# Kernel optimization log

Measured on AMD Instinct MI355X. Metric: run time of the kernel, lower is better.

The kernel has to match this reference:

```python
import jax, jax.numpy as jnp
import numpy as np

K_DIM = 1024
HEADS = 16


def setup_inputs() -> dict:
    key = jax.random.key(0)
    ks = jax.random.split(key, 6)
    b, t, k = 2, 2048, K_DIM
    scale = 1.0 / np.sqrt(k)
    x = jax.random.normal(ks[0], (b, t, k), dtype=jnp.float32)
    # nn.Linear stores weight as [out, in]; y = x @ W.T
    Wq = jax.random.normal(ks[1], (k, k), dtype=jnp.float32) * scale
    Wk = jax.random.normal(ks[2], (k, k), dtype=jnp.float32) * scale
    Wv = jax.random.normal(ks[3], (k, k), dtype=jnp.float32) * scale
    Wo = jax.random.normal(ks[4], (k, k), dtype=jnp.float32) * scale
    bo = jax.random.normal(ks[5], (k,), dtype=jnp.float32) * scale
    return {"x": x, "Wq": Wq, "Wk": Wk, "Wv": Wv, "Wo": Wo, "bo": bo}


def reference(x, Wq, Wk, Wv, Wo, bo):
    b, t, k = x.shape
    h = HEADS
    hd = k // h
    q = (x @ Wq.T).reshape(b, t, h, hd)
    kk = (x @ Wk.T).reshape(b, t, h, hd)
    v = (x @ Wv.T).reshape(b, t, h, hd)
    # scores: [b, h, t, t]
    scores = jnp.einsum('bqhd,bkhd->bhqk', q, kk) / jnp.sqrt(jnp.float32(hd))
    w = jax.nn.softmax(scores, axis=-1)
    out = jnp.einsum('bhqk,bkhd->bqhd', w, v).reshape(b, t, k)
    return out @ Wo.T + bo
```

## Files before the change

kernel.cpp:

```cpp
#include <hip/hip_runtime.h>
#include <stdint.h>
#include <stddef.h>

#define TB 2048
#define KDIM 1024
#define NH 16
#define HD 64

typedef __attribute__((ext_vector_type(8))) __bf16 bf16x8;
typedef __attribute__((ext_vector_type(2))) float f32x2;
typedef __attribute__((ext_vector_type(4))) float f32x4;
typedef __attribute__((ext_vector_type(16))) float f32x16;
typedef __attribute__((ext_vector_type(4))) unsigned short u16x4;
typedef __attribute__((ext_vector_type(8))) unsigned short u16x8;
typedef __attribute__((ext_vector_type(4))) unsigned u32x4;
typedef __attribute__((ext_vector_type(2))) unsigned u32x2;

static __device__ __forceinline__ unsigned short f2bf(float f) {
  unsigned u = __builtin_bit_cast(unsigned, f);
  return (unsigned short)((u + 0x7FFFu + ((u >> 16) & 1u)) >> 16);
}

static __device__ __forceinline__ bf16x8 ld_frag(const unsigned short* p) {
  u16x8 v = *(const u16x8*)p;
  return __builtin_bit_cast(bf16x8, v);
}

static __device__ __forceinline__ void gload_lds16(const void* g, void* l) {
  auto gp = (const __attribute__((address_space(1))) unsigned int*)(uintptr_t)g;
  auto lp = (__attribute__((address_space(3))) unsigned int*)(unsigned int)(uintptr_t)l;
  __builtin_amdgcn_global_load_lds(gp, lp, 16, 0, 0);
}

static __device__ __forceinline__ float fast_exp2(float x) {
  float r;
  asm("v_exp_f32 %0, %1" : "=v"(r) : "v"(x));
  return r;
}

static __device__ __forceinline__ unsigned cvt_pk(float a, float b) {
  unsigned r;
  asm("v_cvt_pk_bf16_f32 %0, %1, %2" : "=v"(r) : "v"(a), "v"(b));
  return r;
}

static __device__ __forceinline__ u32x2 permswap(unsigned a, unsigned b) {
  return __builtin_amdgcn_permlane32_swap(a, b, false, false);
}

static __device__ __forceinline__ f32x2 pk_fma(f32x2 a, f32x2 b, f32x2 c) {
  f32x2 d;
  asm("v_pk_fma_f32 %0, %1, %2, %3" : "=v"(d) : "v"(a), "v"(b), "v"(c));
  return d;
}
static __device__ __forceinline__ f32x2 pk_add(f32x2 a, f32x2 b) {
  f32x2 d;
  asm("v_pk_add_f32 %0, %1, %2" : "=v"(d) : "v"(a), "v"(b));
  return d;
}

__global__ __launch_bounds__(256) void k_cvt_all(
    const float* __restrict__ x, const float* __restrict__ Wq,
    const float* __restrict__ Wk, const float* __restrict__ Wv,
    const float* __restrict__ Wo, unsigned short* __restrict__ xb,
    unsigned short* __restrict__ wb) {
  int bb = blockIdx.x;
  const float* src;
  unsigned short* dst;
  int i;
  if (bb < 2048) {
    src = x; dst = xb; i = bb * 256 + threadIdx.x;
  } else {
    int wsel = (bb - 2048) >> 9;
    src = (wsel == 0) ? Wq : (wsel == 1) ? Wk : (wsel == 2) ? Wv : Wo;
    dst = wb + (size_t)wsel * (KDIM * KDIM);
    i = ((bb - 2048) & 511) * 256 + threadIdx.x;
  }
  const float4* p = (const float4*)src + (size_t)i * 2;
  float4 a = p[0], b = p[1];
  u16x8 o;
  o[0] = f2bf(a.x); o[1] = f2bf(a.y); o[2] = f2bf(a.z); o[3] = f2bf(a.w);
  o[4] = f2bf(b.x); o[5] = f2bf(b.y); o[6] = f2bf(b.z); o[7] = f2bf(b.w);
  *((u16x8*)dst + i) = o;
}

template <int MODE>
static __device__ __forceinline__ void gemm_body(
    const unsigned short* __restrict__ A, const unsigned short* __restrict__ W,
    unsigned short* __restrict__ Cb, float* __restrict__ Cf,
    const float* __restrict__ bias, int by, int bx,
    unsigned short* As, unsigned short* Bs) {
  const int K = KDIM, N = KDIM;
  int tid = threadIdx.x, lane = tid & 63, wid = tid >> 6;
  int r = lane & 15, g = lane >> 4;
  int wm = wid >> 1, wn = wid & 1;

  f32x4 acc[4][4];
#pragma unroll
  for (int m = 0; m < 4; ++m)
#pragma unroll
    for (int n = 0; n < 4; ++n) acc[m][n] = (f32x4){0.f, 0.f, 0.f, 0.f};

  const unsigned short* Ag = A + (size_t)(by * 128) * K;
  const unsigned short* Wg = W + (size_t)(bx * 128) * K;

  for (int k0 = 0; k0 < K; k0 += 64) {
#pragma unroll
    for (int it = 0; it < 4; ++it) {
      int base = it * 256 + wid * 64;
      int c = base + lane;
      int rr = c >> 3;
      int blk = (c & 7) ^ (rr & 7);
      gload_lds16(Ag + (size_t)rr * K + k0 + blk * 8, &As[base * 8]);
      gload_lds16(Wg + (size_t)rr * K + k0 + blk * 8, &Bs[base * 8]);
    }
    __syncthreads();
#pragma unroll
    for (int ks = 0; ks < 2; ++ks) {
      bf16x8 af[4], bf[4];
#pragma unroll
      for (int m = 0; m < 4; ++m) {
        int row = wm * 64 + m * 16 + r;
        af[m] = ld_frag(&As[row * 64 + ((ks * 4 + g) ^ (r & 7)) * 8]);
      }
#pragma unroll
      for (int n = 0; n < 4; ++n) {
        int row = wn * 64 + n * 16 + r;
        bf[n] = ld_frag(&Bs[row * 64 + ((ks * 4 + g) ^ (r & 7)) * 8]);
      }
      __builtin_amdgcn_s_setprio(1);
#pragma unroll
      for (int m = 0; m < 4; ++m)
#pragma unroll
        for (int n = 0; n < 4; ++n)
          acc[m][n] = __builtin_amdgcn_mfma_f32_16x16x32_bf16(af[m], bf[n], acc[m][n], 0, 0, 0);
      __builtin_amdgcn_s_setprio(0);
    }
    __syncthreads();
  }

#pragma unroll
  for (int m = 0; m < 4; ++m)
#pragma unroll
    for (int n = 0; n < 4; ++n) {
      int col = bx * 128 + wn * 64 + n * 16 + r;
      if (MODE == 2) {
        int hq = col >> 6, dq = col & 63;
        int row0 = by * 128 + wm * 64 + m * 16 + g * 4;
        int bq = row0 >> 11, tq = row0 & 2047;
        u16x4 pv;
#pragma unroll
        for (int j = 0; j < 4; ++j) pv[j] = f2bf(acc[m][n][j]);
        *(u16x4*)&Cb[(((size_t)(bq * NH + hq)) * HD + dq) * TB + tq] = pv;
      } else {
#pragma unroll
        for (int j = 0; j < 4; ++j) {
          int row = by * 128 + wm * 64 + m * 16 + g * 4 + j;
          if (MODE == 0)
            Cb[(size_t)row * N + col] = f2bf(acc[m][n][j]);
          else
            Cf[(size_t)row * N + col] = acc[m][n][j] + bias[col];
        }
      }
    }
}

__global__ __launch_bounds__(256) void k_gemm_qkv(
    const unsigned short* __restrict__ X,
    const unsigned short* __restrict__ Wq, const unsigned short* __restrict__ Wk,
    const unsigned short* __restrict__ Wv,
    unsigned short* __restrict__ Q, unsigned short* __restrict__ Kp,
    unsigned short* __restrict__ Vt) {
  __shared__ __align__(16) unsigned short As[8192];
  __shared__ __align__(16) unsigned short Bs[8192];
  int bidx = blockIdx.x;
  int xcd = bidx & 7, slot = bidx >> 3;
  int by = xcd * 4 + slot / 24;
  int bxx = slot % 24;
  int which = bxx >> 3, bx = bxx & 7;
  if (which == 2) {
    gemm_body<2>(X, Wv, Vt, nullptr, nullptr, by, bx, As, Bs);
  } else {
    const unsigned short* W = which ? Wk : Wq;
    unsigned short* C = which ? Kp : Q;
    gemm_body<0>(X, W, C, nullptr, nullptr, by, bx, As, Bs);
  }
}

__global__ __launch_bounds__(256) void k_gemm_out(
    const unsigned short* __restrict__ AO, const unsigned short* __restrict__ Wo,
    float* __restrict__ out, const float* __restrict__ bias) {
  __shared__ __align__(16) unsigned short As[8192];
  __shared__ __align__(16) unsigned short Bs[8192];
  int bidx = blockIdx.x;
  int xcd = bidx & 7, slot = bidx >> 3;
  int by = xcd * 4 + slot / 8;
  int bx = slot & 7;
  gemm_body<1>(AO, Wo, nullptr, out, bias, by, bx, As, Bs);
}

__global__ __launch_bounds__(512, 4) void k_attn(
    const unsigned short* __restrict__ Q, const unsigned short* __restrict__ Kp,
    const unsigned short* __restrict__ Vt, unsigned short* __restrict__ AO) {
  __shared__ __align__(16) unsigned short LDSb[6 * 4096];
  unsigned short* KsB = LDSb;
  unsigned short* VsB = LDSb + 3 * 4096;

  int qt = blockIdx.x >> 5, bh = blockIdx.x & 31;
  int b = bh >> 4, h = bh & 15;
  int tid = threadIdx.x, lane = tid & 63, w = tid >> 6;
  int wl = w & 3, kh = w >> 2;
  int q = lane & 31, hh = lane >> 5;
  const float LOG2E = 1.44269504f;
  const int NT = TB / 64;

  const unsigned short* Qp =
      Q + ((size_t)(b * TB + qt * 128 + wl * 32 + q)) * KDIM + h * HD;
  bf16x8 qf[4];
#pragma unroll
  for (int f = 0; f < 4; ++f) qf[f] = ld_frag(&Qp[16 * f + 8 * hh]);

  f32x16 o0, o1;
#pragma unroll
  for (int i = 0; i < 16; ++i) { o0[i] = 0.f; o1[i] = 0.f; }
  float l_run = 0.f;

  int c = w * 64 + lane;
  int rr = c >> 3;
  int blk = (c & 7) ^ (rr & 7);
  const unsigned short* Kg =
      Kp + (size_t)(b * TB) * KDIM + h * HD + (size_t)rr * KDIM + blk * 8;
  const unsigned short* Vg =
      Vt + (size_t)bh * HD * TB + (size_t)rr * TB + blk * 8;
  int ldst = w * 512;

  auto stage = [&](int kt, int buf) {
    gload_lds16(Kg + (size_t)kt * 64 * KDIM, &KsB[buf * 4096 + ldst]);
    gload_lds16(Vg + kt * 64, &VsB[buf * 4096 + ldst]);
  };

  stage(0, 0);
  stage(1, 1);
  asm volatile("s_waitcnt vmcnt(2)" ::: "memory");
  __builtin_amdgcn_s_barrier();
  __builtin_amdgcn_sched_barrier(0);

  const float c1 = 0.125f * LOG2E;
  const float c2 = 10.0f * LOG2E;
  f32x2 c1v; c1v[0] = c1; c1v[1] = c1;
  f32x2 c2v; c2v[0] = -c2; c2v[1] = -c2;

  for (int t = 0; t < NT; ++t) {
    int cur = t % 3;
    bool pf = (t + 2 < NT);
    if (pf) stage(t + 2, (t + 2) % 3);

    const unsigned short* Kc = &KsB[cur * 4096];
    f32x16 st;
#pragma unroll
    for (int i = 0; i < 16; ++i) st[i] = 0.f;
    __builtin_amdgcn_s_setprio(1);
#pragma unroll
    for (int f = 0; f < 4; ++f) {
      int row = kh * 32 + q;
      int bl = (2 * f + hh) ^ (q & 7);
      bf16x8 kf = ld_frag(&Kc[row * 64 + bl * 8]);
      st = __builtin_amdgcn_mfma_f32_32x32x16_bf16(kf, qf[f], st, 0, 0, 0);
    }
    __builtin_amdgcn_s_setprio(0);

    f32x2 rsv; rsv[0] = 0.f; rsv[1] = 0.f;
    unsigned d[8];
#pragma unroll
    for (int i = 0; i < 8; ++i) {
      f32x2 p; p[0] = st[2 * i]; p[1] = st[2 * i + 1];
      p = pk_fma(p, c1v, c2v);
      f32x2 e; e[0] = fast_exp2(p[0]); e[1] = fast_exp2(p[1]);
      rsv = pk_add(rsv, e);
      d[i] = cvt_pk(e[0], e[1]);
    }
    u32x2 r1 = permswap(d[0], d[2]);
    u32x2 r2 = permswap(d[1], d[3]);
    u32x2 r3 = permswap(d[4], d[6]);
    u32x2 r4 = permswap(d[5], d[7]);
    u32x4 t0; t0[0] = r1.x; t0[1] = r2.x; t0[2] = r1.y; t0[3] = r2.y;
    u32x4 t1; t1[0] = r3.x; t1[1] = r4.x; t1[2] = r3.y; t1[3] = r4.y;
    bf16x8 pa0 = __builtin_bit_cast(bf16x8, t0);
    bf16x8 pa1 = __builtin_bit_cast(bf16x8, t1);
    float rs = rsv[0] + rsv[1];
    rs += __shfl_xor(rs, 32);
    l_run += rs;

    const unsigned short* Vc = &VsB[cur * 4096];
    __builtin_amdgcn_s_setprio(1);
    {
      int bl0 = (kh * 4 + hh) ^ (q & 7);
      int bl1 = (kh * 4 + 2 + hh) ^ (q & 7);
      bf16x8 v00 = ld_frag(&Vc[q * 64 + bl0 * 8]);
      bf16x8 v01 = ld_frag(&Vc[(32 + q) * 64 + bl0 * 8]);
      bf16x8 v10 = ld_frag(&Vc[q * 64 + bl1 * 8]);
      bf16x8 v11 = ld_frag(&Vc[(32 + q) * 64 + bl1 * 8]);
      o0 = __builtin_amdgcn_mfma_f32_32x32x16_bf16(pa0, v00, o0, 0, 0, 0);
      o1 = __builtin_amdgcn_mfma_f32_32x32x16_bf16(pa0, v01, o1, 0, 0, 0);
      o0 = __builtin_amdgcn_mfma_f32_32x32x16_bf16(pa1, v10, o0, 0, 0, 0);
      o1 = __builtin_amdgcn_mfma_f32_32x32x16_bf16(pa1, v11, o1, 0, 0, 0);
    }
    __builtin_amdgcn_s_setprio(0);

    if (pf) asm volatile("s_waitcnt vmcnt(2)" ::: "memory");
    else    asm volatile("s_waitcnt vmcnt(0)" ::: "memory");
    __builtin_amdgcn_s_barrier();
    __builtin_amdgcn_sched_barrier(0);
  }

  float* Osw = (float*)LDSb;
  float* MLb = ((float*)LDSb) + 8192;
  if (kh) {
#pragma unroll
    for (int p = 0; p < 16; ++p) {
      Osw[p * 256 + wl * 64 + lane]        = o0[p];
      Osw[(16 + p) * 256 + wl * 64 + lane] = o1[p];
    }
    if (!hh) MLb[wl * 32 + q] = l_run;
  }
  __syncthreads();
  if (!kh) {
    float il = 1.f / (l_run + MLb[wl * 32 + q]);
#pragma unroll
    for (int p = 0; p < 16; ++p) {
      int qr = (p & 3) + 8 * (p >> 2) + 4 * hh;
      float ip = __shfl(il, qr);
      float v0 = (o0[p] + Osw[p * 256 + wl * 64 + lane]) * ip;
      float v1 = (o1[p] + Osw[(16 + p) * 256 + wl * 64 + lane]) * ip;
      int row = qt * 128 + wl * 32 + qr;
      size_t base = ((size_t)(b * TB + row)) * KDIM + h * HD;
      AO[base + q]      = f2bf(v0);
      AO[base + 32 + q] = f2bf(v1);
    }
  }
}

extern "C" void kernel_launch(void* const* d_in, const int* in_sizes, int n_in,
                              void* d_out, int out_size, void* d_ws, size_t ws_size,
                              hipStream_t stream) {
  const float* x  = (const float*)d_in[0];
  const float* Wq = (const float*)d_in[1];
  const float* Wk = (const float*)d_in[2];
  const float* Wv = (const float*)d_in[3];
  const float* Wo = (const float*)d_in[4];
  const float* bo = (const float*)d_in[5];

  char* ws = (char*)d_ws;
  const size_t MB = 1 << 20;
  unsigned short* xb  = (unsigned short*)(ws + 0 * MB);
  unsigned short* wqb = (unsigned short*)(ws + 8 * MB);
  unsigned short* wkb = (unsigned short*)(ws + 10 * MB);
  unsigned short* wvb = (unsigned short*)(ws + 12 * MB);
  unsigned short* wob = (unsigned short*)(ws + 14 * MB);
  unsigned short* Qb  = (unsigned short*)(ws + 16 * MB);
  unsigned short* Kb  = (unsigned short*)(ws + 24 * MB);
  unsigned short* Vtb = (unsigned short*)(ws + 32 * MB);
  unsigned short* AOb = (unsigned short*)(ws + 40 * MB);

  k_cvt_all<<<4096, 256, 0, stream>>>(x, Wq, Wk, Wv, Wo, xb, wqb);
  k_gemm_qkv<<<32 * 24, 256, 0, stream>>>(xb, wqb, wkb, wvb, Qb, Kb, Vtb);
  k_attn<<<512, 512, 0, stream>>>(Qb, Kb, Vtb, AOb);
  k_gemm_out<<<256, 256, 0, stream>>>(AOb, wob, (float*)d_out, bo);
}
```

Before: 114.0 us.

## Split attention KV range across two blocks and merge partials in a new kernel

The attention kernel now splits each (batch, head, query-tile) over two halves of the key sequence, launching 1024 blocks instead of 512. Each block writes unnormalised fp32 partial outputs and row sums to workspace, and a new merge kernel sums them, normalises and converts to bf16. This raises parallelism to fill more CUs and waves per CU, at the cost of extra global traffic for the partials and an additional launch. It relies on the softmax using a fixed max offset rather than a running max, so the partials can simply be added.

```diff
diff --git a/kernel.cpp b/kernel.cpp
--- a/kernel.cpp
+++ b/kernel.cpp
@@ -201,18 +201,21 @@
 
 __global__ __launch_bounds__(512, 4) void k_attn(
     const unsigned short* __restrict__ Q, const unsigned short* __restrict__ Kp,
-    const unsigned short* __restrict__ Vt, unsigned short* __restrict__ AO) {
+    const unsigned short* __restrict__ Vt,
+    float* __restrict__ Opart, float* __restrict__ lpart) {
   __shared__ __align__(16) unsigned short LDSb[6 * 4096];
   unsigned short* KsB = LDSb;
   unsigned short* VsB = LDSb + 3 * 4096;
 
-  int qt = blockIdx.x >> 5, bh = blockIdx.x & 31;
+  int bidx = blockIdx.x;
+  int bh = bidx & 31, qt = (bidx >> 5) & 15, half = bidx >> 9;
   int b = bh >> 4, h = bh & 15;
   int tid = threadIdx.x, lane = tid & 63, w = tid >> 6;
   int wl = w & 3, kh = w >> 2;
   int q = lane & 31, hh = lane >> 5;
   const float LOG2E = 1.44269504f;
-  const int NT = TB / 64;
+  const int NTH = 16;
+  int kt0 = half * NTH;
 
   const unsigned short* Qp =
       Q + ((size_t)(b * TB + qt * 128 + wl * 32 + q)) * KDIM + h * HD;
@@ -234,7 +237,8 @@
       Vt + (size_t)bh * HD * TB + (size_t)rr * TB + blk * 8;
   int ldst = w * 512;
 
-  auto stage = [&](int kt, int buf) {
+  auto stage = [&](int t, int buf) {
+    int kt = kt0 + t;
     gload_lds16(Kg + (size_t)kt * 64 * KDIM, &KsB[buf * 4096 + ldst]);
     gload_lds16(Vg + kt * 64, &VsB[buf * 4096 + ldst]);
   };
@@ -250,9 +254,9 @@
   f32x2 c1v; c1v[0] = c1; c1v[1] = c1;
   f32x2 c2v; c2v[0] = -c2; c2v[1] = -c2;
 
-  for (int t = 0; t < NT; ++t) {
+  for (int t = 0; t < NTH; ++t) {
     int cur = t % 3;
-    bool pf = (t + 2 < NT);
+    bool pf = (t + 2 < NTH);
     if (pf) stage(t + 2, (t + 2) % 3);
 
     const unsigned short* Kc = &KsB[cur * 4096];
@@ -314,7 +318,7 @@
   }
 
   float* Osw = (float*)LDSb;
-  float* MLb = ((float*)LDSb) + 8192;
+  float* MLb = Osw + 8192;
   if (kh) {
 #pragma unroll
     for (int p = 0; p < 16; ++p) {
@@ -324,19 +328,50 @@
     if (!hh) MLb[wl * 32 + q] = l_run;
   }
   __syncthreads();
+
+  int pair = bh * 16 + qt;
+  size_t pbase = ((size_t)(pair * 2 + half)) * 8192;
   if (!kh) {
-    float il = 1.f / (l_run + MLb[wl * 32 + q]);
+    float l_tot = l_run + MLb[wl * 32 + q];
 #pragma unroll
     for (int p = 0; p < 16; ++p) {
       int qr = (p & 3) + 8 * (p >> 2) + 4 * hh;
-      float ip = __shfl(il, qr);
-      float v0 = (o0[p] + Osw[p * 256 + wl * 64 + lane]) * ip;
-      float v1 = (o1[p] + Osw[(16 + p) * 256 + wl * 64 + lane]) * ip;
-      int row = qt * 128 + wl * 32 + qr;
-      size_t base = ((size_t)(b * TB + row)) * KDIM + h * HD;
-      AO[base + q]      = f2bf(v0);
-      AO[base + 32 + q] = f2bf(v1);
-    }
+      float v0 = o0[p] + Osw[p * 256 + wl * 64 + lane];
+      float v1 = o1[p] + Osw[(16 + p) * 256 + wl * 64 + lane];
+      int row = wl * 32 + qr;
+      Opart[pbase + row * 64 + q]      = v0;
+      Opart[pbase + row * 64 + 32 + q] = v1;
+    }
+    if (!hh) lpart[(size_t)(pair * 2 + half) * 128 + wl * 32 + q] = l_tot;
+  }
+}
+
+__global__ __launch_bounds__(256) void k_merge(
+    const float* __restrict__ Opart, const float* __restrict__ lpart,
+    unsigned short* __restrict__ AO) {
+  int bidx = blockIdx.x;
+  int pair = bidx >> 1, rh = bidx & 1;
+  int bh = pair >> 4, qt = pair & 15;
+  int b = bh >> 4, h = bh & 15;
+  int tid = threadIdx.x;
+  int c0 = (tid & 15) * 4;
+  size_t p0 = (size_t)(pair * 2) * 8192;
+  size_t p1 = p0 + 8192;
+  const float* la = lpart + (size_t)(pair * 2) * 128;
+  const float* lb = la + 128;
+#pragma unroll
+  for (int it = 0; it < 4; ++it) {
+    int rr = rh * 64 + it * 16 + (tid >> 4);
+    float il = 1.f / (la[rr] + lb[rr]);
+    float4 a = *(const float4*)&Opart[p0 + rr * 64 + c0];
+    float4 bv = *(const float4*)&Opart[p1 + rr * 64 + c0];
+    u16x4 o;
+    o[0] = f2bf((a.x + bv.x) * il);
+    o[1] = f2bf((a.y + bv.y) * il);
+    o[2] = f2bf((a.z + bv.z) * il);
+    o[3] = f2bf((a.w + bv.w) * il);
+    int grow = qt * 128 + rr;
+    *(u16x4*)&AO[((size_t)(b * TB + grow)) * KDIM + h * HD + c0] = o;
   }
 }
 
@@ -361,9 +396,12 @@
   unsigned short* Kb  = (unsigned short*)(ws + 24 * MB);
   unsigned short* Vtb = (unsigned short*)(ws + 32 * MB);
   unsigned short* AOb = (unsigned short*)(ws + 40 * MB);
+  float* Opart = (float*)(ws + 48 * MB);
+  float* lpart = (float*)(ws + 80 * MB);
 
   k_cvt_all<<<4096, 256, 0, stream>>>(x, Wq, Wk, Wv, Wo, xb, wqb);
   k_gemm_qkv<<<32 * 24, 256, 0, stream>>>(xb, wqb, wkb, wvb, Qb, Kb, Vtb);
-  k_attn<<<512, 512, 0, stream>>>(Qb, Kb, Vtb, AOb);
+  k_attn<<<1024, 512, 0, stream>>>(Qb, Kb, Vtb, Opart, lpart);
+  k_merge<<<1024, 256, 0, stream>>>(Opart, lpart, AOb);
   k_gemm_out<<<256, 256, 0, stream>>>(AOb, wob, (float*)d_out, bo);
 }
```

Result: slower. 123.3 us (+8.1%).

## Double-buffer attention K/V in two-tile chunks to halve barriers

Applied to the files above, without the earlier changes.

The attention key loop now processes two 64-key tiles per iteration. It double-buffers 128-key chunks of K and V in LDS, replacing the earlier triple-buffered pipeline that synchronised after every tile. The goal is fewer workgroup barriers and waitcnt stalls per key, with larger prefetch batches. In exchange, LDS per block grows from 48 KB to 64 KB, which can lower the number of resident blocks per CU. Each iteration also waits for all outstanding loads (vmcnt(0)), so there is less slack to overlap loads with compute.

```diff
diff --git a/kernel.cpp b/kernel.cpp
--- a/kernel.cpp
+++ b/kernel.cpp
@@ -202,9 +202,9 @@
 __global__ __launch_bounds__(512, 4) void k_attn(
     const unsigned short* __restrict__ Q, const unsigned short* __restrict__ Kp,
     const unsigned short* __restrict__ Vt, unsigned short* __restrict__ AO) {
-  __shared__ __align__(16) unsigned short LDSb[6 * 4096];
+  __shared__ __align__(16) unsigned short LDSb[8 * 4096];
   unsigned short* KsB = LDSb;
-  unsigned short* VsB = LDSb + 3 * 4096;
+  unsigned short* VsB = LDSb + 4 * 4096;
 
   int qt = blockIdx.x >> 5, bh = blockIdx.x & 31;
   int b = bh >> 4, h = bh & 15;
@@ -212,7 +212,7 @@
   int wl = w & 3, kh = w >> 2;
   int q = lane & 31, hh = lane >> 5;
   const float LOG2E = 1.44269504f;
-  const int NT = TB / 64;
+  const int NU = 16;
 
   const unsigned short* Qp =
       Q + ((size_t)(b * TB + qt * 128 + wl * 32 + q)) * KDIM + h * HD;
@@ -234,14 +234,18 @@
       Vt + (size_t)bh * HD * TB + (size_t)rr * TB + blk * 8;
   int ldst = w * 512;
 
-  auto stage = [&](int kt, int buf) {
-    gload_lds16(Kg + (size_t)kt * 64 * KDIM, &KsB[buf * 4096 + ldst]);
-    gload_lds16(Vg + kt * 64, &VsB[buf * 4096 + ldst]);
+  auto stage = [&](int u, int buf) {
+#pragma unroll
+    for (int tt = 0; tt < 2; ++tt) {
+      int kt = u * 2 + tt;
+      int slot = buf * 2 + tt;
+      gload_lds16(Kg + (size_t)kt * 64 * KDIM, &KsB[slot * 4096 + ldst]);
+      gload_lds16(Vg + kt * 64, &VsB[slot * 4096 + ldst]);
+    }
   };
 
   stage(0, 0);
-  stage(1, 1);
-  asm volatile("s_waitcnt vmcnt(2)" ::: "memory");
+  asm volatile("s_waitcnt vmcnt(0)" ::: "memory");
   __builtin_amdgcn_s_barrier();
   __builtin_amdgcn_sched_barrier(0);
 
@@ -250,71 +254,73 @@
   f32x2 c1v; c1v[0] = c1; c1v[1] = c1;
   f32x2 c2v; c2v[0] = -c2; c2v[1] = -c2;
 
-  for (int t = 0; t < NT; ++t) {
-    int cur = t % 3;
-    bool pf = (t + 2 < NT);
-    if (pf) stage(t + 2, (t + 2) % 3);
-
-    const unsigned short* Kc = &KsB[cur * 4096];
-    f32x16 st;
-#pragma unroll
-    for (int i = 0; i < 16; ++i) st[i] = 0.f;
-    __builtin_amdgcn_s_setprio(1);
-#pragma unroll
-    for (int f = 0; f < 4; ++f) {
-      int row = kh * 32 + q;
-      int bl = (2 * f + hh) ^ (q & 7);
-      bf16x8 kf = ld_frag(&Kc[row * 64 + bl * 8]);
-      st = __builtin_amdgcn_mfma_f32_32x32x16_bf16(kf, qf[f], st, 0, 0, 0);
-    }
-    __builtin_amdgcn_s_setprio(0);
-
-    f32x2 rsv; rsv[0] = 0.f; rsv[1] = 0.f;
-    unsigned d[8];
-#pragma unroll
-    for (int i = 0; i < 8; ++i) {
-      f32x2 p; p[0] = st[2 * i]; p[1] = st[2 * i + 1];
-      p = pk_fma(p, c1v, c2v);
-      f32x2 e; e[0] = fast_exp2(p[0]); e[1] = fast_exp2(p[1]);
-      rsv = pk_add(rsv, e);
-      d[i] = cvt_pk(e[0], e[1]);
-    }
-    u32x2 r1 = permswap(d[0], d[2]);
-    u32x2 r2 = permswap(d[1], d[3]);
-    u32x2 r3 = permswap(d[4], d[6]);
-    u32x2 r4 = permswap(d[5], d[7]);
-    u32x4 t0; t0[0] = r1.x; t0[1] = r2.x; t0[2] = r1.y; t0[3] = r2.y;
-    u32x4 t1; t1[0] = r3.x; t1[1] = r4.x; t1[2] = r3.y; t1[3] = r4.y;
-    bf16x8 pa0 = __builtin_bit_cast(bf16x8, t0);
-    bf16x8 pa1 = __builtin_bit_cast(bf16x8, t1);
-    float rs = rsv[0] + rsv[1];
-    rs += __shfl_xor(rs, 32);
-    l_run += rs;
-
-    const unsigned short* Vc = &VsB[cur * 4096];
-    __builtin_amdgcn_s_setprio(1);
-    {
-      int bl0 = (kh * 4 + hh) ^ (q & 7);
-      int bl1 = (kh * 4 + 2 + hh) ^ (q & 7);
-      bf16x8 v00 = ld_frag(&Vc[q * 64 + bl0 * 8]);
-      bf16x8 v01 = ld_frag(&Vc[(32 + q) * 64 + bl0 * 8]);
-      bf16x8 v10 = ld_frag(&Vc[q * 64 + bl1 * 8]);
-      bf16x8 v11 = ld_frag(&Vc[(32 + q) * 64 + bl1 * 8]);
-      o0 = __builtin_amdgcn_mfma_f32_32x32x16_bf16(pa0, v00, o0, 0, 0, 0);
-      o1 = __builtin_amdgcn_mfma_f32_32x32x16_bf16(pa0, v01, o1, 0, 0, 0);
-      o0 = __builtin_amdgcn_mfma_f32_32x32x16_bf16(pa1, v10, o0, 0, 0, 0);
-      o1 = __builtin_amdgcn_mfma_f32_32x32x16_bf16(pa1, v11, o1, 0, 0, 0);
-    }
-    __builtin_amdgcn_s_setprio(0);
-
-    if (pf) asm volatile("s_waitcnt vmcnt(2)" ::: "memory");
-    else    asm volatile("s_waitcnt vmcnt(0)" ::: "memory");
+  for (int u = 0; u < NU; ++u) {
+    int buf = u & 1;
+    if (u + 1 < NU) stage(u + 1, buf ^ 1);
+
+#pragma unroll
+    for (int tt = 0; tt < 2; ++tt) {
+      int slot = buf * 2 + tt;
+      const unsigned short* Kc = &KsB[slot * 4096];
+      f32x16 st;
+#pragma unroll
+      for (int i = 0; i < 16; ++i) st[i] = 0.f;
+      __builtin_amdgcn_s_setprio(1);
+#pragma unroll
+      for (int f = 0; f < 4; ++f) {
+        int row = kh * 32 + q;
+        int bl = (2 * f + hh) ^ (q & 7);
+        bf16x8 kf = ld_frag(&Kc[row * 64 + bl * 8]);
+        st = __builtin_amdgcn_mfma_f32_32x32x16_bf16(kf, qf[f], st, 0, 0, 0);
+      }
+      __builtin_amdgcn_s_setprio(0);
+
+      f32x2 rsv; rsv[0] = 0.f; rsv[1] = 0.f;
+      unsigned d[8];
+#pragma unroll
+      for (int i = 0; i < 8; ++i) {
+        f32x2 p; p[0] = st[2 * i]; p[1] = st[2 * i + 1];
+        p = pk_fma(p, c1v, c2v);
+        f32x2 e; e[0] = fast_exp2(p[0]); e[1] = fast_exp2(p[1]);
+        rsv = pk_add(rsv, e);
+        d[i] = cvt_pk(e[0], e[1]);
+      }
+      u32x2 r1 = permswap(d[0], d[2]);
+      u32x2 r2 = permswap(d[1], d[3]);
+      u32x2 r3 = permswap(d[4], d[6]);
+      u32x2 r4 = permswap(d[5], d[7]);
+      u32x4 t0; t0[0] = r1.x; t0[1] = r2.x; t0[2] = r1.y; t0[3] = r2.y;
+      u32x4 t1; t1[0] = r3.x; t1[1] = r4.x; t1[2] = r3.y; t1[3] = r4.y;
+      bf16x8 pa0 = __builtin_bit_cast(bf16x8, t0);
+      bf16x8 pa1 = __builtin_bit_cast(bf16x8, t1);
+      float rs = rsv[0] + rsv[1];
+      rs += __shfl_xor(rs, 32);
+      l_run += rs;
+
+      const unsigned short* Vc = &VsB[slot * 4096];
+      __builtin_amdgcn_s_setprio(1);
+      {
+        int bl0 = (kh * 4 + hh) ^ (q & 7);
+        int bl1 = (kh * 4 + 2 + hh) ^ (q & 7);
+        bf16x8 v00 = ld_frag(&Vc[q * 64 + bl0 * 8]);
+        bf16x8 v01 = ld_frag(&Vc[(32 + q) * 64 + bl0 * 8]);
+        bf16x8 v10 = ld_frag(&Vc[q * 64 + bl1 * 8]);
+        bf16x8 v11 = ld_frag(&Vc[(32 + q) * 64 + bl1 * 8]);
+        o0 = __builtin_amdgcn_mfma_f32_32x32x16_bf16(pa0, v00, o0, 0, 0, 0);
+        o1 = __builtin_amdgcn_mfma_f32_32x32x16_bf16(pa0, v01, o1, 0, 0, 0);
+        o0 = __builtin_amdgcn_mfma_f32_32x32x16_bf16(pa1, v10, o0, 0, 0, 0);
+        o1 = __builtin_amdgcn_mfma_f32_32x32x16_bf16(pa1, v11, o1, 0, 0, 0);
+      }
+      __builtin_amdgcn_s_setprio(0);
+    }
+
+    asm volatile("s_waitcnt vmcnt(0)" ::: "memory");
     __builtin_amdgcn_s_barrier();
     __builtin_amdgcn_sched_barrier(0);
   }
 
   float* Osw = (float*)LDSb;
-  float* MLb = ((float*)LDSb) + 8192;
+  float* MLb = Osw + 8192;
   if (kh) {
 #pragma unroll
     for (int p = 0; p < 16; ++p) {
```

After: 112.4 us. About the same (-1.5%).
